# Kernel tuning notes

Hardware: AMD Instinct MI355X
Metric: run time of the kernel (lower is better)

Reference implementation:

```python
import jax, jax.numpy as jnp
import numpy as np

IN_DIM = 6
OUT_DIM = 6
H = 512
OUT_LEN = 256


def _lstm_cell(x, h, c, Wih, Whh, bih, bhh):
    # torch gate order: i, f, g, o
    gates = x @ Wih.T + h @ Whh.T + bih + bhh  # (B, 4H)
    i, f, g, o = jnp.split(gates, 4, axis=-1)
    i = jax.nn.sigmoid(i)
    f = jax.nn.sigmoid(f)
    g = jnp.tanh(g)
    o = jax.nn.sigmoid(o)
    c2 = f * c + i * g
    h2 = o * jnp.tanh(c2)
    return h2, c2


def _lstm_layer(x_seq, Wih, Whh, bih, bhh):
    # x_seq: (T, B, Din) -> (y_seq (T,B,H), h_T (B,H), c_T (B,H))
    B = x_seq.shape[1]
    Hs = Whh.shape[1]
    h0 = jnp.zeros((B, Hs), x_seq.dtype)
    c0 = jnp.zeros((B, Hs), x_seq.dtype)

    def step(carry, x):
        h, c = carry
        h2, c2 = _lstm_cell(x, h, c, Wih, Whh, bih, bhh)
        return (h2, c2), h2

    (hT, cT), ys = jax.lax.scan(step, (h0, c0), x_seq)
    return ys, hT, cT


def setup_inputs() -> dict:
    key = jax.random.key(0)
    ks = jax.random.split(key, 32)
    bound = 1.0 / np.sqrt(H)
    u = lambda k, shape: jax.random.uniform(k, shape, jnp.float32, -bound, bound)
    inp = {"src": jax.random.normal(ks[0], (128, 256, IN_DIM), jnp.float32)}
    # encoder layer 0 / 1
    inp["enc_Wih0"] = u(ks[1], (4 * H, IN_DIM)); inp["enc_Whh0"] = u(ks[2], (4 * H, H))
    inp["enc_bih0"] = u(ks[3], (4 * H,));       inp["enc_bhh0"] = u(ks[4], (4 * H,))
    inp["enc_Wih1"] = u(ks[5], (4 * H, H));     inp["enc_Whh1"] = u(ks[6], (4 * H, H))
    inp["enc_bih1"] = u(ks[7], (4 * H,));       inp["enc_bhh1"] = u(ks[8], (4 * H,))
    # decoder layer 0 / 1
    inp["dec_Wih0"] = u(ks[9], (4 * H, OUT_DIM)); inp["dec_Whh0"] = u(ks[10], (4 * H, H))
    inp["dec_bih0"] = u(ks[11], (4 * H,));        inp["dec_bhh0"] = u(ks[12], (4 * H,))
    inp["dec_Wih1"] = u(ks[13], (4 * H, H));      inp["dec_Whh1"] = u(ks[14], (4 * H, H))
    inp["dec_bih1"] = u(ks[15], (4 * H,));        inp["dec_bhh1"] = u(ks[16], (4 * H,))
    # decoder output head
    inp["fc_W"] = u(ks[17], (OUT_DIM, H))
    inp["fc_b"] = u(ks[18], (OUT_DIM,))
    return inp


def reference(src,
              enc_Wih0, enc_Whh0, enc_bih0, enc_bhh0,
              enc_Wih1, enc_Whh1, enc_bih1, enc_bhh1,
              dec_Wih0, dec_Whh0, dec_bih0, dec_bhh0,
              dec_Wih1, dec_Whh1, dec_bih1, dec_bhh1,
              fc_W, fc_b):
    # ---- encoder: 2-layer unidirectional LSTM over src ----
    x = jnp.transpose(src, (1, 0, 2))  # (Tin, B, 6)
    y0, h0, c0 = _lstm_layer(x, enc_Wih0, enc_Whh0, enc_bih0, enc_bhh0)
    _, h1, c1 = _lstm_layer(y0, enc_Wih1, enc_Whh1, enc_bih1, enc_bhh1)
    # bridge: Henc==Hdec, unidirectional -> identity

    def dec_step(carry, _):
        inp_t, dh0, dc0, dh1, dc1 = carry
        dh0, dc0 = _lstm_cell(inp_t, dh0, dc0, dec_Wih0, dec_Whh0, dec_bih0, dec_bhh0)
        dh1, dc1 = _lstm_cell(dh0, dh1, dc1, dec_Wih1, dec_Whh1, dec_bih1, dec_bhh1)
        out_t = dh1 @ fc_W.T + fc_b  # (B, 6)
        return (out_t, dh0, dc0, dh1, dc1), out_t

    init = (src[:, -1, :], h0, c0, h1, c1)
    _, outs = jax.lax.scan(dec_step, init, None, length=OUT_LEN)
    return jnp.transpose(outs, (1, 0, 2))  # (B, OUT_LEN, 6)
```

## Files before the change

kernel.cpp:

```cpp
#include <hip/hip_runtime.h>
#include <hip/hip_fp16.h>

struct P19 {
  const float *src;
  const float *eWih0, *eWhh0, *ebih0, *ebhh0;
  const float *eWih1, *eWhh1, *ebih1, *ebhh1;
  const float *dWih0, *dWhh0, *dbih0, *dbhh0;
  const float *dWih1, *dWhh1, *dbih1, *dbhh1;
  const float *fcW, *fcb;
  float *out;
  float *ws;
};

typedef _Float16 h2v __attribute__((ext_vector_type(2)));

__device__ __forceinline__ float sigf(float x) { return 1.f / (1.f + __expf(-x)); }

__device__ __forceinline__ unsigned packh(float a, float b2) {
  __half2 h2 = __floats2half2_rn(a, b2);
  return *(const unsigned *)&h2;
}

__device__ __forceinline__ unsigned ldh(const unsigned *p) {
  return __hip_atomic_load((const unsigned *)p, __ATOMIC_RELAXED, __HIP_MEMORY_SCOPE_AGENT);
}
__device__ __forceinline__ void sth(unsigned *p, unsigned v) {
  __hip_atomic_store(p, v, __ATOMIC_RELAXED, __HIP_MEMORY_SCOPE_AGENT);
}
__device__ __forceinline__ void sthf(float *p, float v) {
  __hip_atomic_store(p, v, __ATOMIC_RELAXED, __HIP_MEMORY_SCOPE_AGENT);
}
__device__ __forceinline__ float ldhf(const float *p) {
  return __hip_atomic_load((const float *)p, __ATOMIC_RELAXED, __HIP_MEMORY_SCOPE_AGENT);
}

__device__ __forceinline__ float dot2(unsigned h, unsigned w, float acc) {
#if __has_builtin(__builtin_amdgcn_fdot2)
  return __builtin_amdgcn_fdot2(*(h2v *)&h, *(h2v *)&w, acc, false);
#else
  float2 hf = __half22float2(*(const __half2 *)&h);
  float2 wf = __half22float2(*(const __half2 *)&w);
  return fmaf(hf.x, wf.x, fmaf(hf.y, wf.y, acc));
#endif
}

__device__ __forceinline__ void arrive(unsigned *flags, unsigned gen, int tid, int blk) {
  __syncthreads();
  if (tid == 0) sth(flags + blk * 32, gen);
}
__device__ __forceinline__ void waitbar(unsigned *flags, unsigned gen, int tid) {
  {
    unsigned *f = flags + tid * 32;
    int g = 0;
    while (ldh(f) < gen) {
      __builtin_amdgcn_s_sleep(8);
      if (++g > (1 << 16)) break;
    }
  }
  __syncthreads();
}

__device__ __forceinline__ void dotq1(float *A, const uint4 *__restrict__ wq,
                                      const unsigned *__restrict__ hq) {
  unsigned ca[32], cb[32];
#pragma unroll
  for (int c = 0; c < 32; ++c) ca[c] = ldh(hq + c * 128);
  for (int j = 0; j < 4; j += 2) {
#pragma unroll
    for (int c = 0; c < 32; ++c) cb[c] = ldh(hq + ((j + 1) * 32 + c) * 128);
#pragma unroll
    for (int c = 0; c < 32; ++c) {
      int k2 = j * 32 + c;
      uint4 w0 = wq[k2 * 2], w1 = wq[k2 * 2 + 1];
      unsigned h = ca[c];
      A[0] = dot2(h, w0.x, A[0]); A[1] = dot2(h, w0.y, A[1]);
      A[2] = dot2(h, w0.z, A[2]); A[3] = dot2(h, w0.w, A[3]);
      A[4] = dot2(h, w1.x, A[4]); A[5] = dot2(h, w1.y, A[5]);
      A[6] = dot2(h, w1.z, A[6]); A[7] = dot2(h, w1.w, A[7]);
    }
#pragma unroll
    for (int c = 0; c < 32; ++c) ca[c] = ldh(hq + ((((j + 2) & 3)) * 32 + c) * 128);
#pragma unroll
    for (int c = 0; c < 32; ++c) {
      int k2 = (j + 1) * 32 + c;
      uint4 w0 = wq[k2 * 2], w1 = wq[k2 * 2 + 1];
      unsigned h = cb[c];
      A[0] = dot2(h, w0.x, A[0]); A[1] = dot2(h, w0.y, A[1]);
      A[2] = dot2(h, w0.z, A[2]); A[3] = dot2(h, w0.w, A[3]);
      A[4] = dot2(h, w1.x, A[4]); A[5] = dot2(h, w1.y, A[5]);
      A[6] = dot2(h, w1.z, A[6]); A[7] = dot2(h, w1.w, A[7]);
    }
  }
}
__device__ __forceinline__ void dotq2(float *A, const uint4 *__restrict__ w0q,
                                      const uint4 *__restrict__ w1q,
                                      const unsigned *__restrict__ hq) {
  unsigned ca[32], cb[32];
#pragma unroll
  for (int c = 0; c < 32; ++c) ca[c] = ldh(hq + c * 128);
  for (int j = 0; j < 4; j += 2) {
#pragma unroll
    for (int c = 0; c < 32; ++c) cb[c] = ldh(hq + ((j + 1) * 32 + c) * 128);
#pragma unroll
    for (int c = 0; c < 32; ++c) {
      int k2 = j * 32 + c;
      uint4 a0 = w0q[k2 * 2], a1 = w0q[k2 * 2 + 1];
      uint4 b0 = w1q[k2 * 2], b1 = w1q[k2 * 2 + 1];
      unsigned h = ca[c];
      A[0] = dot2(h, a0.x, A[0]);   A[1] = dot2(h, a0.y, A[1]);
      A[2] = dot2(h, a0.z, A[2]);   A[3] = dot2(h, a0.w, A[3]);
      A[4] = dot2(h, a1.x, A[4]);   A[5] = dot2(h, a1.y, A[5]);
      A[6] = dot2(h, a1.z, A[6]);   A[7] = dot2(h, a1.w, A[7]);
      A[8] = dot2(h, b0.x, A[8]);   A[9] = dot2(h, b0.y, A[9]);
      A[10] = dot2(h, b0.z, A[10]); A[11] = dot2(h, b0.w, A[11]);
      A[12] = dot2(h, b1.x, A[12]); A[13] = dot2(h, b1.y, A[13]);
      A[14] = dot2(h, b1.z, A[14]); A[15] = dot2(h, b1.w, A[15]);
    }
#pragma unroll
    for (int c = 0; c < 32; ++c) ca[c] = ldh(hq + ((((j + 2) & 3)) * 32 + c) * 128);
#pragma unroll
    for (int c = 0; c < 32; ++c) {
      int k2 = (j + 1) * 32 + c;
      uint4 a0 = w0q[k2 * 2], a1 = w0q[k2 * 2 + 1];
      uint4 b0 = w1q[k2 * 2], b1 = w1q[k2 * 2 + 1];
      unsigned h = cb[c];
      A[0] = dot2(h, a0.x, A[0]);   A[1] = dot2(h, a0.y, A[1]);
      A[2] = dot2(h, a0.z, A[2]);   A[3] = dot2(h, a0.w, A[3]);
      A[4] = dot2(h, a1.x, A[4]);   A[5] = dot2(h, a1.y, A[5]);
      A[6] = dot2(h, a1.z, A[6]);   A[7] = dot2(h, a1.w, A[7]);
      A[8] = dot2(h, b0.x, A[8]);   A[9] = dot2(h, b0.y, A[9]);
      A[10] = dot2(h, b0.z, A[10]); A[11] = dot2(h, b0.w, A[11]);
      A[12] = dot2(h, b1.x, A[12]); A[13] = dot2(h, b1.y, A[13]);
      A[14] = dot2(h, b1.z, A[14]); A[15] = dot2(h, b1.w, A[15]);
    }
  }
}

__device__ __forceinline__ void fc_emit(const unsigned *__restrict__ h1buf,
                                        const float *__restrict__ fcW,
                                        const float *__restrict__ fcb,
                                        float *__restrict__ out, int sIdx,
                                        int tid, int blk) {
  int q = tid >> 6, l = tid & 63;
  if (q < 3) {
    int o = blk * 3 + q, j = o >> 7, bb = o & 127;
    const unsigned *hc = h1buf + bb;
    const float2 *fw = (const float2 *)(fcW + j * 512);
    float acc = 0.f;
#pragma unroll
    for (int r = 0; r < 4; ++r) {
      int k2 = l + r * 64;
      unsigned d = ldh(hc + k2 * 128);
      float2 hf = __half22float2(*(const __half2 *)&d);
      float2 wv = fw[k2];
      acc = fmaf(wv.x, hf.x, acc);
      acc = fmaf(wv.y, hf.y, acc);
    }
#pragma unroll
    for (int off = 32; off; off >>= 1) acc += __shfl_down(acc, off, 64);
    if (l == 0) out[((size_t)bb * 256 + sIdx) * 6 + j] = acc + fcb[j];
  }
}

__global__ __launch_bounds__(256, 1) void seq2seq_kernel(P19 p) {
  const int tid = threadIdx.x;
  const int blk = blockIdx.x;
  const int b = tid & 127;
  const int kh = tid >> 7;

  float *ws = p.ws;
  unsigned *flags = (unsigned *)ws;
  unsigned *hpB = (unsigned *)(ws + 8256);
  unsigned *hp0r[2] = {hpB, hpB + 32768};
  unsigned *hp1r[2] = {hpB + 65536, hpB + 98304};
  float *outp = ws + 8256 + 131072;
  float *srcT = outp + 768;

  __shared__ __align__(16) uint4 wl4[3584];
  __shared__ float4 redux[6][128];
  __shared__ float wxe[48], wxd[48], bbuf[40];
  unsigned *wl1 = (unsigned *)wl4;

  {
    const float *mats[6] = {p.eWhh0, p.eWih1, p.eWhh1, p.dWhh0, p.dWih1, p.dWhh1};
    for (int e = tid; e < 12288; e += 256) {
      int k2 = e & 255, r = e >> 8;
      int g = r & 3, uu = (r >> 2) & 1, m = r >> 3;
      const float *row = mats[m] + (size_t)(g * 512 + blk * 2 + uu) * 512;
      wl1[(m * 512 + k2 * 2 + uu) * 4 + g] = packh(row[2 * k2], row[2 * k2 + 1]);
    }
    for (int e = tid; e < 2048; e += 256) {
      int uu = e >> 10, rem = e & 1023, g = rem & 3, k2 = rem >> 2;
      const float *wr = p.dWih0 + (size_t)(g * 512 + blk * 2 + uu) * 6;
      float v0 = 0.f, v1 = 0.f;
#pragma unroll
      for (int i = 0; i < 6; ++i) {
        v0 = fmaf(wr[i], p.fcW[i * 512 + 2 * k2], v0);
        v1 = fmaf(wr[i], p.fcW[i * 512 + 2 * k2 + 1], v1);
      }
      wl1[(6 * 512 + k2 * 2 + uu) * 4 + g] = packh(v0, v1);
    }
    if (tid < 40) {
      int f = tid >> 3, k = tid & 7, uu = k >> 2, g = k & 3;
      int r2 = g * 512 + blk * 2 + uu;
      float v;
      if (f == 0) v = p.ebih0[r2] + p.ebhh0[r2];
      else if (f == 1) v = p.ebih1[r2] + p.ebhh1[r2];
      else if (f == 2) v = p.dbih1[r2] + p.dbhh1[r2];
      else {
        v = p.dbih0[r2] + p.dbhh0[r2];
        if (f == 3)
#pragma unroll
          for (int i = 0; i < 6; ++i) v = fmaf(p.dWih0[(size_t)r2 * 6 + i], p.fcb[i], v);
      }
      bbuf[tid] = v;
    } else if (tid >= 64 && tid < 112) {
      int idx = tid - 64, uu = idx / 24, rem = idx % 24, g = rem / 6, i = rem % 6;
      wxe[idx] = p.eWih0[(size_t)(g * 512 + blk * 2 + uu) * 6 + i];
    } else if (tid >= 128 && tid < 176) {
      int idx = tid - 128, uu = idx / 24, rem = idx % 24, g = rem / 6, i = rem % 6;
      wxd[idx] = p.dWih0[(size_t)(g * 512 + blk * 2 + uu) * 6 + i];
    }
  }
  for (int e = blk * 256 + tid; e < 196608; e += 65536) {
    int bb = e & 127, rest = e >> 7, i = rest % 6, t = rest / 6;
    sthf(&srcT[t * 768 + i * 128 + bb], p.src[((size_t)bb * 256 + t) * 6 + i]);
  }
  {
    int g0 = blk * 256 + tid;
    if (g0 < 768) {
      int bb = g0 & 127, i = g0 >> 7;
      sthf(&outp[i * 128 + bb], p.src[((size_t)bb * 256 + 255) * 6 + i]);
    }
  }
  float c0[2] = {0.f, 0.f}, c1[2] = {0.f, 0.f};
  unsigned gen = 1;
  arrive(flags, gen, tid, blk);
  waitbar(flags, gen, tid);

#define WQ(m) (wl4 + (m) * 512 + kh * 256)
#define HST(buf) ((const unsigned *)(buf) + kh * 16384 + b)
#define RADD(gb, slot) { float4 v = redux[slot][b]; \
    G[(gb)] += v.x; G[(gb) + 1] += v.y; G[(gb) + 2] += v.z; G[(gb) + 3] += v.w; }

  for (int t = 0; t <= 256; ++t) {
    float A16[16], A8[8];
#pragma unroll
    for (int i = 0; i < 16; ++i) A16[i] = 0.f;
#pragma unroll
    for (int i = 0; i < 8; ++i) A8[i] = 0.f;
    dotq2(A16, WQ(0), WQ(1), HST(hp0r[t & 1]));
    dotq1(A8, WQ(2), HST(hp1r[(t + 1) & 1]));
    if (kh) {
      redux[0][b] = make_float4(A16[0], A16[1], A16[2], A16[3]);
      redux[1][b] = make_float4(A16[4], A16[5], A16[6], A16[7]);
      redux[2][b] = make_float4(A16[8], A16[9], A16[10], A16[11]);
      redux[3][b] = make_float4(A16[12], A16[13], A16[14], A16[15]);
      redux[4][b] = make_float4(A8[0], A8[1], A8[2], A8[3]);
      redux[5][b] = make_float4(A8[4], A8[5], A8[6], A8[7]);
    }
    __syncthreads();
    if (kh == 0) {
      float G[24];
#pragma unroll
      for (int i = 0; i < 16; ++i) G[i] = A16[i];
#pragma unroll
      for (int i = 0; i < 8; ++i) G[16 + i] = A8[i];
      { RADD(0, 0) RADD(4, 1) RADD(8, 2) RADD(12, 3) RADD(16, 4) RADD(20, 5) }
      if (t < 256) {
        float xv[6], h0v[2];
#pragma unroll
        for (int i = 0; i < 6; ++i) xv[i] = srcT[t * 768 + i * 128 + b];
#pragma unroll
        for (int uu = 0; uu < 2; ++uu) {
          float g4[4];
#pragma unroll
          for (int g = 0; g < 4; ++g) {
            float v = G[uu * 4 + g] + bbuf[uu * 4 + g];
#pragma unroll
            for (int i = 0; i < 6; ++i) v = fmaf(wxe[uu * 24 + g * 6 + i], xv[i], v);
            g4[g] = v;
          }
          float ig = sigf(g4[0]), fg = sigf(g4[1]), gg = tanhf(g4[2]), og = sigf(g4[3]);
          c0[uu] = fg * c0[uu] + ig * gg;
          h0v[uu] = og * tanhf(c0[uu]);
        }
        sth(&hp0r[(t + 1) & 1][blk * 128 + b], packh(h0v[0], h0v[1]));
      }
      if (t >= 1) {
        float h1v[2];
#pragma unroll
        for (int uu = 0; uu < 2; ++uu) {
          float g4[4];
#pragma unroll
          for (int g = 0; g < 4; ++g)
            g4[g] = G[8 + uu * 4 + g] + G[16 + uu * 4 + g] + bbuf[8 + uu * 4 + g];
          float ig = sigf(g4[0]), fg = sigf(g4[1]), gg = tanhf(g4[2]), og = sigf(g4[3]);
          c1[uu] = fg * c1[uu] + ig * gg;
          h1v[uu] = og * tanhf(c1[uu]);
        }
        sth(&hp1r[t & 1][blk * 128 + b], packh(h1v[0], h1v[1]));
      }
    }
    arrive(flags, ++gen, tid, blk);
    waitbar(flags, gen, tid);
  }

  for (int s = 0; s < 256; ++s) {
    float A3[8];
#pragma unroll
    for (int i = 0; i < 8; ++i) A3[i] = 0.f;
    dotq1(A3, WQ(3), HST(hp0r[s & 1]));
    if (s) waitbar(flags, gen, tid);
    float AA[16];
#pragma unroll
    for (int i = 0; i < 16; ++i) AA[i] = 0.f;
    if (s == 0) {
      dotq1(AA + 8, WQ(5), HST(hp1r[0]));
    } else {
      dotq2(AA, WQ(6), WQ(5), HST(hp1r[s & 1]));
      fc_emit(hp1r[s & 1], p.fcW, p.fcb, p.out, s - 1, tid, blk);
    }
    if (kh) {
      redux[0][b] = make_float4(A3[0], A3[1], A3[2], A3[3]);
      redux[1][b] = make_float4(A3[4], A3[5], A3[6], A3[7]);
      redux[2][b] = make_float4(AA[0], AA[1], AA[2], AA[3]);
      redux[3][b] = make_float4(AA[4], AA[5], AA[6], AA[7]);
    }
    __syncthreads();
    if (kh == 0) {
      float G[8];
#pragma unroll
      for (int i = 0; i < 8; ++i) G[i] = A3[i] + AA[i];
      { RADD(0, 0) RADD(4, 1) RADD(0, 2) RADD(4, 3) }
      float bq[8];
      if (s == 0) {
        float xv[6];
#pragma unroll
        for (int i = 0; i < 6; ++i) xv[i] = ldhf(&outp[i * 128 + b]);
#pragma unroll
        for (int k = 0; k < 8; ++k) {
          int uu = k >> 2, g = k & 3;
          float v = bbuf[32 + k];
#pragma unroll
          for (int i = 0; i < 6; ++i) v = fmaf(wxd[uu * 24 + g * 6 + i], xv[i], v);
          bq[k] = v;
        }
      } else {
#pragma unroll
        for (int k = 0; k < 8; ++k) bq[k] = bbuf[24 + k];
      }
      float h0v[2];
#pragma unroll
      for (int uu = 0; uu < 2; ++uu) {
        float ig = sigf(G[uu * 4 + 0] + bq[uu * 4 + 0]);
        float fg = sigf(G[uu * 4 + 1] + bq[uu * 4 + 1]);
        float gg = tanhf(G[uu * 4 + 2] + bq[uu * 4 + 2]);
        float og = sigf(G[uu * 4 + 3] + bq[uu * 4 + 3]);
        c0[uu] = fg * c0[uu] + ig * gg;
        h0v[uu] = og * tanhf(c0[uu]);
      }
      sth(&hp0r[(s + 1) & 1][blk * 128 + b], packh(h0v[0], h0v[1]));
    }
    arrive(flags, ++gen, tid, blk);
    waitbar(flags, gen, tid);
    float A4[8];
#pragma unroll
    for (int i = 0; i < 8; ++i) A4[i] = AA[8 + i];
    dotq1(A4, WQ(4), HST(hp0r[(s + 1) & 1]));
    if (kh) {
      redux[0][b] = make_float4(A4[0], A4[1], A4[2], A4[3]);
      redux[1][b] = make_float4(A4[4], A4[5], A4[6], A4[7]);
    }
    __syncthreads();
    if (kh == 0) {
      float G[8];
#pragma unroll
      for (int i = 0; i < 8; ++i) G[i] = A4[i];
      { RADD(0, 0) RADD(4, 1) }
      float h1v[2];
#pragma unroll
      for (int uu = 0; uu < 2; ++uu) {
        float ig = sigf(G[uu * 4 + 0] + bbuf[16 + uu * 4 + 0]);
        float fg = sigf(G[uu * 4 + 1] + bbuf[16 + uu * 4 + 1]);
        float gg = tanhf(G[uu * 4 + 2] + bbuf[16 + uu * 4 + 2]);
        float og = sigf(G[uu * 4 + 3] + bbuf[16 + uu * 4 + 3]);
        c1[uu] = fg * c1[uu] + ig * gg;
        h1v[uu] = og * tanhf(c1[uu]);
      }
      sth(&hp1r[(s + 1) & 1][blk * 128 + b], packh(h1v[0], h1v[1]));
    }
    arrive(flags, ++gen, tid, blk);
  }
  waitbar(flags, gen, tid);
  fc_emit(hp1r[0], p.fcW, p.fcb, p.out, 255, tid, blk);
}

extern "C" void kernel_launch(void *const *d_in, const int *in_sizes, int n_in,
                              void *d_out, int out_size, void *d_ws, size_t ws_size,
                              hipStream_t stream) {
  (void)in_sizes; (void)n_in; (void)out_size; (void)ws_size;
  P19 p;
  p.src = (const float *)d_in[0];
  p.eWih0 = (const float *)d_in[1];  p.eWhh0 = (const float *)d_in[2];
  p.ebih0 = (const float *)d_in[3];  p.ebhh0 = (const float *)d_in[4];
  p.eWih1 = (const float *)d_in[5];  p.eWhh1 = (const float *)d_in[6];
  p.ebih1 = (const float *)d_in[7];  p.ebhh1 = (const float *)d_in[8];
  p.dWih0 = (const float *)d_in[9];  p.dWhh0 = (const float *)d_in[10];
  p.dbih0 = (const float *)d_in[11]; p.dbhh0 = (const float *)d_in[12];
  p.dWih1 = (const float *)d_in[13]; p.dWhh1 = (const float *)d_in[14];
  p.dbih1 = (const float *)d_in[15]; p.dbhh1 = (const float *)d_in[16];
  p.fcW = (const float *)d_in[17];   p.fcb = (const float *)d_in[18];
  p.out = (float *)d_out;
  p.ws = (float *)d_ws;

  hipMemsetAsync(d_ws, 0, (size_t)(8256 + 4 * 32768) * sizeof(float), stream);
  seq2seq_kernel<<<dim3(256), dim3(256), 0, stream>>>(p);
}
```

Measured before the change: 12.39 ms.

## Remap threads to two batch elements per lane with four-way K split

Each thread now handles two batch columns using 64-bit hidden-state loads, and the K dimension is split across four wavefronts instead of two. Partial sums are reduced through a new shared buffer, with different wavefronts finishing the layer-0 and layer-1 cells so the two run in parallel. The grid barrier wait now polls with a single wavefront checking four flags per lane. The aim is to reuse each weight load across two batch elements and cut global load and barrier traffic, at the cost of more registers and a three-way shared-memory reduction.

Result: slower. 27.52 ms (+122.0%).

```diff
diff --git a/kernel.cpp b/kernel.cpp
--- a/kernel.cpp
+++ b/kernel.cpp
@@ -22,7 +22,7 @@
 }
 
 __device__ __forceinline__ unsigned ldh(const unsigned *p) {
-  return __hip_atomic_load((const unsigned *)p, __ATOMIC_RELAXED, __HIP_MEMORY_SCOPE_AGENT);
+  return __hip_atomic_load(p, __ATOMIC_RELAXED, __HIP_MEMORY_SCOPE_AGENT);
 }
 __device__ __forceinline__ void sth(unsigned *p, unsigned v) {
   __hip_atomic_store(p, v, __ATOMIC_RELAXED, __HIP_MEMORY_SCOPE_AGENT);
@@ -30,8 +30,20 @@
 __device__ __forceinline__ void sthf(float *p, float v) {
   __hip_atomic_store(p, v, __ATOMIC_RELAXED, __HIP_MEMORY_SCOPE_AGENT);
 }
-__device__ __forceinline__ float ldhf(const float *p) {
-  return __hip_atomic_load((const float *)p, __ATOMIC_RELAXED, __HIP_MEMORY_SCOPE_AGENT);
+__device__ __forceinline__ uint2 ldh2(const unsigned *p) {
+  unsigned long long v = __hip_atomic_load((const unsigned long long *)p,
+                                           __ATOMIC_RELAXED, __HIP_MEMORY_SCOPE_AGENT);
+  uint2 r; r.x = (unsigned)v; r.y = (unsigned)(v >> 32); return r;
+}
+__device__ __forceinline__ void sth2(unsigned *p, unsigned lo, unsigned hi) {
+  unsigned long long v = ((unsigned long long)hi << 32) | (unsigned long long)lo;
+  __hip_atomic_store((unsigned long long *)p, v, __ATOMIC_RELAXED, __HIP_MEMORY_SCOPE_AGENT);
+}
+__device__ __forceinline__ float2 ldhf2(const float *p) {
+  union { unsigned long long u; float2 f; } c;
+  c.u = __hip_atomic_load((const unsigned long long *)p, __ATOMIC_RELAXED,
+                          __HIP_MEMORY_SCOPE_AGENT);
+  return c.f;
 }
 
 __device__ __forceinline__ float dot2(unsigned h, unsigned w, float acc) {
@@ -49,91 +61,119 @@
   if (tid == 0) sth(flags + blk * 32, gen);
 }
 __device__ __forceinline__ void waitbar(unsigned *flags, unsigned gen, int tid) {
-  {
-    unsigned *f = flags + tid * 32;
-    int g = 0;
-    while (ldh(f) < gen) {
-      __builtin_amdgcn_s_sleep(8);
+  if ((tid >> 6) == 3) {
+    int l = tid & 63, g = 0;
+    for (;;) {
+      unsigned a = ldh(flags + (4 * l + 0) * 32);
+      unsigned b = ldh(flags + (4 * l + 1) * 32);
+      unsigned c = ldh(flags + (4 * l + 2) * 32);
+      unsigned d = ldh(flags + (4 * l + 3) * 32);
+      if (min(min(a, b), min(c, d)) >= gen) break;
+      __builtin_amdgcn_s_sleep(4);
       if (++g > (1 << 16)) break;
     }
   }
   __syncthreads();
 }
 
-__device__ __forceinline__ void dotq1(float *A, const uint4 *__restrict__ wq,
+#define DOT8(B, h, w0, w1) {                                          \
+  (B)[0] = dot2(h.x, w0.x, (B)[0]);   (B)[1] = dot2(h.y, w0.x, (B)[1]);   \
+  (B)[2] = dot2(h.x, w0.y, (B)[2]);   (B)[3] = dot2(h.y, w0.y, (B)[3]);   \
+  (B)[4] = dot2(h.x, w0.z, (B)[4]);   (B)[5] = dot2(h.y, w0.z, (B)[5]);   \
+  (B)[6] = dot2(h.x, w0.w, (B)[6]);   (B)[7] = dot2(h.y, w0.w, (B)[7]);   \
+  (B)[8] = dot2(h.x, w1.x, (B)[8]);   (B)[9] = dot2(h.y, w1.x, (B)[9]);   \
+  (B)[10] = dot2(h.x, w1.y, (B)[10]); (B)[11] = dot2(h.y, w1.y, (B)[11]); \
+  (B)[12] = dot2(h.x, w1.z, (B)[12]); (B)[13] = dot2(h.y, w1.z, (B)[13]); \
+  (B)[14] = dot2(h.x, w1.w, (B)[14]); (B)[15] = dot2(h.y, w1.w, (B)[15]); }
+
+__device__ __forceinline__ void dotp1(float *A, const uint4 *__restrict__ wq,
                                       const unsigned *__restrict__ hq) {
-  unsigned ca[32], cb[32];
-#pragma unroll
-  for (int c = 0; c < 32; ++c) ca[c] = ldh(hq + c * 128);
+  uint2 ca[16], cb[16];
+#pragma unroll
+  for (int c = 0; c < 16; ++c) ca[c] = ldh2(hq + c * 128);
   for (int j = 0; j < 4; j += 2) {
 #pragma unroll
-    for (int c = 0; c < 32; ++c) cb[c] = ldh(hq + ((j + 1) * 32 + c) * 128);
-#pragma unroll
-    for (int c = 0; c < 32; ++c) {
-      int k2 = j * 32 + c;
+    for (int c = 0; c < 16; ++c) cb[c] = ldh2(hq + ((j + 1) * 16 + c) * 128);
+#pragma unroll
+    for (int c = 0; c < 16; ++c) {
+      int k2 = j * 16 + c;
       uint4 w0 = wq[k2 * 2], w1 = wq[k2 * 2 + 1];
-      unsigned h = ca[c];
-      A[0] = dot2(h, w0.x, A[0]); A[1] = dot2(h, w0.y, A[1]);
-      A[2] = dot2(h, w0.z, A[2]); A[3] = dot2(h, w0.w, A[3]);
-      A[4] = dot2(h, w1.x, A[4]); A[5] = dot2(h, w1.y, A[5]);
-      A[6] = dot2(h, w1.z, A[6]); A[7] = dot2(h, w1.w, A[7]);
-    }
-#pragma unroll
-    for (int c = 0; c < 32; ++c) ca[c] = ldh(hq + ((((j + 2) & 3)) * 32 + c) * 128);
-#pragma unroll
-    for (int c = 0; c < 32; ++c) {
-      int k2 = (j + 1) * 32 + c;
+      uint2 h = ca[c];
+      DOT8(A, h, w0, w1)
+    }
+#pragma unroll
+    for (int c = 0; c < 16; ++c) ca[c] = ldh2(hq + ((((j + 2) & 3)) * 16 + c) * 128);
+#pragma unroll
+    for (int c = 0; c < 16; ++c) {
+      int k2 = (j + 1) * 16 + c;
       uint4 w0 = wq[k2 * 2], w1 = wq[k2 * 2 + 1];
-      unsigned h = cb[c];
-      A[0] = dot2(h, w0.x, A[0]); A[1] = dot2(h, w0.y, A[1]);
-      A[2] = dot2(h, w0.z, A[2]); A[3] = dot2(h, w0.w, A[3]);
-      A[4] = dot2(h, w1.x, A[4]); A[5] = dot2(h, w1.y, A[5]);
-      A[6] = dot2(h, w1.z, A[6]); A[7] = dot2(h, w1.w, A[7]);
-    }
-  }
-}
-__device__ __forceinline__ void dotq2(float *A, const uint4 *__restrict__ w0q,
-                                      const uint4 *__restrict__ w1q,
+      uint2 h = cb[c];
+      DOT8(A, h, w0, w1)
+    }
+  }
+}
+__device__ __forceinline__ void dotp2(float *A , const uint4 *__restrict__ wa,
+                                      const uint4 *__restrict__ wb,
                                       const unsigned *__restrict__ hq) {
-  unsigned ca[32], cb[32];
-#pragma unroll
-  for (int c = 0; c < 32; ++c) ca[c] = ldh(hq + c * 128);
+  uint2 ca[16], cb[16];
+#pragma unroll
+  for (int c = 0; c < 16; ++c) ca[c] = ldh2(hq + c * 128);
   for (int j = 0; j < 4; j += 2) {
 #pragma unroll
-    for (int c = 0; c < 32; ++c) cb[c] = ldh(hq + ((j + 1) * 32 + c) * 128);
-#pragma unroll
-    for (int c = 0; c < 32; ++c) {
-      int k2 = j * 32 + c;
-      uint4 a0 = w0q[k2 * 2], a1 = w0q[k2 * 2 + 1];
-      uint4 b0 = w1q[k2 * 2], b1 = w1q[k2 * 2 + 1];
-      unsigned h = ca[c];
-      A[0] = dot2(h, a0.x, A[0]);   A[1] = dot2(h, a0.y, A[1]);
-      A[2] = dot2(h, a0.z, A[2]);   A[3] = dot2(h, a0.w, A[3]);
-      A[4] = dot2(h, a1.x, A[4]);   A[5] = dot2(h, a1.y, A[5]);
-      A[6] = dot2(h, a1.z, A[6]);   A[7] = dot2(h, a1.w, A[7]);
-      A[8] = dot2(h, b0.x, A[8]);   A[9] = dot2(h, b0.y, A[9]);
-      A[10] = dot2(h, b0.z, A[10]); A[11] = dot2(h, b0.w, A[11]);
-      A[12] = dot2(h, b1.x, A[12]); A[13] = dot2(h, b1.y, A[13]);
-      A[14] = dot2(h, b1.z, A[14]); A[15] = dot2(h, b1.w, A[15]);
-    }
-#pragma unroll
-    for (int c = 0; c < 32; ++c) ca[c] = ldh(hq + ((((j + 2) & 3)) * 32 + c) * 128);
-#pragma unroll
-    for (int c = 0; c < 32; ++c) {
-      int k2 = (j + 1) * 32 + c;
-      uint4 a0 = w0q[k2 * 2], a1 = w0q[k2 * 2 + 1];
-      uint4 b0 = w1q[k2 * 2], b1 = w1q[k2 * 2 + 1];
-      unsigned h = cb[c];
-      A[0] = dot2(h, a0.x, A[0]);   A[1] = dot2(h, a0.y, A[1]);
-      A[2] = dot2(h, a0.z, A[2]);   A[3] = dot2(h, a0.w, A[3]);
-      A[4] = dot2(h, a1.x, A[4]);   A[5] = dot2(h, a1.y, A[5]);
-      A[6] = dot2(h, a1.z, A[6]);   A[7] = dot2(h, a1.w, A[7]);
-      A[8] = dot2(h, b0.x, A[8]);   A[9] = dot2(h, b0.y, A[9]);
-      A[10] = dot2(h, b0.z, A[10]); A[11] = dot2(h, b0.w, A[11]);
-      A[12] = dot2(h, b1.x, A[12]); A[13] = dot2(h, b1.y, A[13]);
-      A[14] = dot2(h, b1.z, A[14]); A[15] = dot2(h, b1.w, A[15]);
-    }
-  }
+    for (int c = 0; c < 16; ++c) cb[c] = ldh2(hq + ((j + 1) * 16 + c) * 128);
+#pragma unroll
+    for (int c = 0; c < 16; ++c) {
+      int k2 = j * 16 + c;
+      uint2 h = ca[c];
+      uint4 w0 = wa[k2 * 2], w1 = wa[k2 * 2 + 1];
+      DOT8(A, h, w0, w1)
+      uint4 v0 = wb[k2 * 2], v1 = wb[k2 * 2 + 1];
+      DOT8(A + 16, h, v0, v1)
+    }
+#pragma unroll
+    for (int c = 0; c < 16; ++c) ca[c] = ldh2(hq + ((((j + 2) & 3)) * 16 + c) * 128);
+#pragma unroll
+    for (int c = 0; c < 16; ++c) {
+      int k2 = (j + 1) * 16 + c;
+      uint2 h = cb[c];
+      uint4 w0 = wa[k2 * 2], w1 = wa[k2 * 2 + 1];
+      DOT8(A, h, w0, w1)
+      uint4 v0 = wb[k2 * 2], v1 = wb[k2 * 2 + 1];
+      DOT8(A + 16, h, v0, v1)
+    }
+  }
+}
+
+__device__ __forceinline__ void rwrite(float *dst, const float *A) {
+#pragma unroll
+  for (int q = 0; q < 4; ++q)
+    *(float4 *)&dst[q * 4] = make_float4(A[q * 4], A[q * 4 + 1], A[q * 4 + 2], A[q * 4 + 3]);
+}
+__device__ __forceinline__ void rread3(float (*B)[64][20], int l, float *G) {
+#pragma unroll
+  for (int wi = 0; wi < 3; ++wi)
+#pragma unroll
+    for (int q = 0; q < 4; ++q) {
+      float4 v = *(const float4 *)&B[wi][l][q * 4];
+      G[q * 4] += v.x; G[q * 4 + 1] += v.y; G[q * 4 + 2] += v.z; G[q * 4 + 3] += v.w;
+    }
+}
+
+__device__ __forceinline__ void cell2(const float *G, float c[2][2], unsigned hv[2]) {
+  float h[2][2];
+#pragma unroll
+  for (int u = 0; u < 2; ++u)
+#pragma unroll
+    for (int p = 0; p < 2; ++p) {
+      float ig = sigf(G[u * 8 + 0 + p]);
+      float fg = sigf(G[u * 8 + 2 + p]);
+      float gg = tanhf(G[u * 8 + 4 + p]);
+      float og = sigf(G[u * 8 + 6 + p]);
+      c[u][p] = fg * c[u][p] + ig * gg;
+      h[u][p] = og * tanhf(c[u][p]);
+    }
+  hv[0] = packh(h[0][0], h[1][0]);
+  hv[1] = packh(h[0][1], h[1][1]);
 }
 
 __device__ __forceinline__ void fc_emit(const unsigned *__restrict__ h1buf,
@@ -165,8 +205,8 @@
 __global__ __launch_bounds__(256, 1) void seq2seq_kernel(P19 p) {
   const int tid = threadIdx.x;
   const int blk = blockIdx.x;
-  const int b = tid & 127;
-  const int kh = tid >> 7;
+  const int w = tid >> 6;
+  const int l = tid & 63;
 
   float *ws = p.ws;
   unsigned *flags = (unsigned *)ws;
@@ -177,7 +217,7 @@
   float *srcT = outp + 768;
 
   __shared__ __align__(16) uint4 wl4[3584];
-  __shared__ float4 redux[6][128];
+  __shared__ __align__(16) float rb[3][3][64][20];
   __shared__ float wxe[48], wxd[48], bbuf[40];
   unsigned *wl1 = (unsigned *)wl4;
 
@@ -233,162 +273,164 @@
       sthf(&outp[i * 128 + bb], p.src[((size_t)bb * 256 + 255) * 6 + i]);
     }
   }
-  float c0[2] = {0.f, 0.f}, c1[2] = {0.f, 0.f};
+  float c0[2][2] = {{0.f, 0.f}, {0.f, 0.f}};
+  float c1[2][2] = {{0.f, 0.f}, {0.f, 0.f}};
   unsigned gen = 1;
   arrive(flags, gen, tid, blk);
   waitbar(flags, gen, tid);
 
-#define WQ(m) (wl4 + (m) * 512 + kh * 256)
-#define HST(buf) ((const unsigned *)(buf) + kh * 16384 + b)
-#define RADD(gb, slot) { float4 v = redux[slot][b]; \
-    G[(gb)] += v.x; G[(gb) + 1] += v.y; G[(gb) + 2] += v.z; G[(gb) + 3] += v.w; }
+#define WQn(m) (wl4 + (m) * 512 + w * 128)
+#define HSTn(buf) ((const unsigned *)(buf) + w * 8192 + 2 * l)
 
   for (int t = 0; t <= 256; ++t) {
-    float A16[16], A8[8];
-#pragma unroll
-    for (int i = 0; i < 16; ++i) A16[i] = 0.f;
-#pragma unroll
-    for (int i = 0; i < 8; ++i) A8[i] = 0.f;
-    dotq2(A16, WQ(0), WQ(1), HST(hp0r[t & 1]));
-    dotq1(A8, WQ(2), HST(hp1r[(t + 1) & 1]));
-    if (kh) {
-      redux[0][b] = make_float4(A16[0], A16[1], A16[2], A16[3]);
-      redux[1][b] = make_float4(A16[4], A16[5], A16[6], A16[7]);
-      redux[2][b] = make_float4(A16[8], A16[9], A16[10], A16[11]);
-      redux[3][b] = make_float4(A16[12], A16[13], A16[14], A16[15]);
-      redux[4][b] = make_float4(A8[0], A8[1], A8[2], A8[3]);
-      redux[5][b] = make_float4(A8[4], A8[5], A8[6], A8[7]);
+    float A2[32], A1[16];
+#pragma unroll
+    for (int i = 0; i < 32; ++i) A2[i] = 0.f;
+#pragma unroll
+    for (int i = 0; i < 16; ++i) A1[i] = 0.f;
+    dotp2(A2, WQn(0), WQn(1), HSTn(hp0r[t & 1]));
+    dotp1(A1, WQn(2), HSTn(hp1r[(t + 1) & 1]));
+    if (w != 0) rwrite(&rb[0][w - 1][l][0], A2);
+    if (w != 2) {
+      int wi = w > 2 ? w - 1 : w;
+      rwrite(&rb[1][wi][l][0], A2 + 16);
+      rwrite(&rb[2][wi][l][0], A1);
     }
     __syncthreads();
-    if (kh == 0) {
-      float G[24];
-#pragma unroll
-      for (int i = 0; i < 16; ++i) G[i] = A16[i];
-#pragma unroll
-      for (int i = 0; i < 8; ++i) G[16 + i] = A8[i];
-      { RADD(0, 0) RADD(4, 1) RADD(8, 2) RADD(12, 3) RADD(16, 4) RADD(20, 5) }
-      if (t < 256) {
-        float xv[6], h0v[2];
-#pragma unroll
-        for (int i = 0; i < 6; ++i) xv[i] = srcT[t * 768 + i * 128 + b];
-#pragma unroll
-        for (int uu = 0; uu < 2; ++uu) {
-          float g4[4];
-#pragma unroll
-          for (int g = 0; g < 4; ++g) {
-            float v = G[uu * 4 + g] + bbuf[uu * 4 + g];
-#pragma unroll
-            for (int i = 0; i < 6; ++i) v = fmaf(wxe[uu * 24 + g * 6 + i], xv[i], v);
-            g4[g] = v;
+    if (w == 0 && t < 256) {
+      float G[16];
+#pragma unroll
+      for (int i = 0; i < 16; ++i) G[i] = A2[i];
+      rread3(rb[0], l, G);
+      float2 xv[6];
+#pragma unroll
+      for (int i = 0; i < 6; ++i)
+        xv[i] = *(const float2 *)&srcT[t * 768 + i * 128 + 2 * l];
+#pragma unroll
+      for (int u = 0; u < 2; ++u)
+#pragma unroll
+        for (int g = 0; g < 4; ++g) {
+          float a0 = bbuf[u * 4 + g], a1 = a0;
+#pragma unroll
+          for (int i = 0; i < 6; ++i) {
+            float wv = wxe[u * 24 + g * 6 + i];
+            a0 = fmaf(wv, xv[i].x, a0);
+            a1 = fmaf(wv, xv[i].y, a1);
           }
-          float ig = sigf(g4[0]), fg = sigf(g4[1]), gg = tanhf(g4[2]), og = sigf(g4[3]);
-          c0[uu] = fg * c0[uu] + ig * gg;
-          h0v[uu] = og * tanhf(c0[uu]);
+          G[u * 8 + g * 2 + 0] += a0;
+          G[u * 8 + g * 2 + 1] += a1;
         }
-        sth(&hp0r[(t + 1) & 1][blk * 128 + b], packh(h0v[0], h0v[1]));
-      }
-      if (t >= 1) {
-        float h1v[2];
-#pragma unroll
-        for (int uu = 0; uu < 2; ++uu) {
-          float g4[4];
-#pragma unroll
-          for (int g = 0; g < 4; ++g)
-            g4[g] = G[8 + uu * 4 + g] + G[16 + uu * 4 + g] + bbuf[8 + uu * 4 + g];
-          float ig = sigf(g4[0]), fg = sigf(g4[1]), gg = tanhf(g4[2]), og = sigf(g4[3]);
-          c1[uu] = fg * c1[uu] + ig * gg;
-          h1v[uu] = og * tanhf(c1[uu]);
+      unsigned hv[2];
+      cell2(G, c0, hv);
+      sth2(&hp0r[(t + 1) & 1][blk * 128 + 2 * l], hv[0], hv[1]);
+    }
+    if (w == 2 && t >= 1) {
+      float G[16];
+#pragma unroll
+      for (int i = 0; i < 16; ++i) G[i] = A2[16 + i] + A1[i];
+      rread3(rb[1], l, G);
+      rread3(rb[2], l, G);
+#pragma unroll
+      for (int u = 0; u < 2; ++u)
+#pragma unroll
+        for (int g = 0; g < 4; ++g) {
+          float bs = bbuf[8 + u * 4 + g];
+          G[u * 8 + g * 2 + 0] += bs;
+          G[u * 8 + g * 2 + 1] += bs;
         }
-        sth(&hp1r[t & 1][blk * 128 + b], packh(h1v[0], h1v[1]));
-      }
+      unsigned hv[2];
+      cell2(G, c1, hv);
+      sth2(&hp1r[t & 1][blk * 128 + 2 * l], hv[0], hv[1]);
     }
     arrive(flags, ++gen, tid, blk);
     waitbar(flags, gen, tid);
   }
 
   for (int s = 0; s < 256; ++s) {
-    float A3[8];
-#pragma unroll
-    for (int i = 0; i < 8; ++i) A3[i] = 0.f;
-    dotq1(A3, WQ(3), HST(hp0r[s & 1]));
+    float A0[16];
+#pragma unroll
+    for (int i = 0; i < 16; ++i) A0[i] = 0.f;
+    dotp1(A0, WQn(3), HSTn(hp0r[s & 1]));
     if (s) waitbar(flags, gen, tid);
-    float AA[16];
-#pragma unroll
-    for (int i = 0; i < 16; ++i) AA[i] = 0.f;
+    float A12[32];
+#pragma unroll
+    for (int i = 0; i < 32; ++i) A12[i] = 0.f;
     if (s == 0) {
-      dotq1(AA + 8, WQ(5), HST(hp1r[0]));
+      dotp1(A12 + 16, WQn(5), HSTn(hp1r[0]));
     } else {
-      dotq2(AA, WQ(6), WQ(5), HST(hp1r[s & 1]));
+      dotp2(A12, WQn(6), WQn(5), HSTn(hp1r[s & 1]));
       fc_emit(hp1r[s & 1], p.fcW, p.fcb, p.out, s - 1, tid, blk);
     }
-    if (kh) {
-      redux[0][b] = make_float4(A3[0], A3[1], A3[2], A3[3]);
-      redux[1][b] = make_float4(A3[4], A3[5], A3[6], A3[7]);
-      redux[2][b] = make_float4(AA[0], AA[1], AA[2], AA[3]);
-      redux[3][b] = make_float4(AA[4], AA[5], AA[6], AA[7]);
+    if (w != 0) {
+      rwrite(&rb[0][w - 1][l][0], A0);
+      rwrite(&rb[1][w - 1][l][0], A12);
     }
     __syncthreads();
-    if (kh == 0) {
-      float G[8];
-#pragma unroll
-      for (int i = 0; i < 8; ++i) G[i] = A3[i] + AA[i];
-      { RADD(0, 0) RADD(4, 1) RADD(0, 2) RADD(4, 3) }
-      float bq[8];
+    if (w == 0) {
+      float G[16];
+#pragma unroll
+      for (int i = 0; i < 16; ++i) G[i] = A0[i] + A12[i];
+      rread3(rb[0], l, G);
+      rread3(rb[1], l, G);
       if (s == 0) {
-        float xv[6];
-#pragma unroll
-        for (int i = 0; i < 6; ++i) xv[i] = ldhf(&outp[i * 128 + b]);
-#pragma unroll
-        for (int k = 0; k < 8; ++k) {
-          int uu = k >> 2, g = k & 3;
-          float v = bbuf[32 + k];
-#pragma unroll
-          for (int i = 0; i < 6; ++i) v = fmaf(wxd[uu * 24 + g * 6 + i], xv[i], v);
-          bq[k] = v;
-        }
+        float2 xv[6];
+#pragma unroll
+        for (int i = 0; i < 6; ++i) xv[i] = ldhf2(&outp[i * 128 + 2 * l]);
+#pragma unroll
+        for (int u = 0; u < 2; ++u)
+#pragma unroll
+          for (int g = 0; g < 4; ++g) {
+            float a0 = bbuf[32 + u * 4 + g], a1 = a0;
+#pragma unroll
+            for (int i = 0; i < 6; ++i) {
+              float wv = wxd[u * 24 + g * 6 + i];
+              a0 = fmaf(wv, xv[i].x, a0);
+              a1 = fmaf(wv, xv[i].y, a1);
+            }
+            G[u * 8 + g * 2 + 0] += a0;
+            G[u * 8 + g * 2 + 1] += a1;
+          }
       } else {
 #pragma unroll
-        for (int k = 0; k < 8; ++k) bq[k] = bbuf[24 + k];
+        for (int u = 0; u < 2; ++u)
+#pragma unroll
+          for (int g = 0; g < 4; ++g) {
+            float bs = bbuf[24 + u * 4 + g];
+            G[u * 8 + g * 2 + 0] += bs;
+            G[u * 8 + g * 2 + 1] += bs;
+          }
       }
-      float h0v[2];
-#pragma unroll
-      for (int uu = 0; uu < 2; ++uu) {
-        float ig = sigf(G[uu * 4 + 0] + bq[uu * 4 + 0]);
-        float fg = sigf(G[uu * 4 + 1] + bq[uu * 4 + 1]);
-        float gg = tanhf(G[uu * 4 + 2] + bq[uu * 4 + 2]);
-        float og = sigf(G[uu * 4 + 3] + bq[uu * 4 + 3]);
-        c0[uu] = fg * c0[uu] + ig * gg;
-        h0v[uu] = og * tanhf(c0[uu]);
-      }
-      sth(&hp0r[(s + 1) & 1][blk * 128 + b], packh(h0v[0], h0v[1]));
+      unsigned hv[2];
+      cell2(G, c0, hv);
+      sth2(&hp0r[(s + 1) & 1][blk * 128 + 2 * l], hv[0], hv[1]);
     }
     arrive(flags, ++gen, tid, blk);
     waitbar(flags, gen, tid);
-    float A4[8];
-#pragma unroll
-    for (int i = 0; i < 8; ++i) A4[i] = AA[8 + i];
-    dotq1(A4, WQ(4), HST(hp0r[(s + 1) & 1]));
-    if (kh) {
-      redux[0][b] = make_float4(A4[0], A4[1], A4[2], A4[3]);
-      redux[1][b] = make_float4(A4[4], A4[5], A4[6], A4[7]);
+    float A4[16];
+#pragma unroll
+    for (int i = 0; i < 16; ++i) A4[i] = A12[16 + i];
+    dotp1(A4, WQn(4), HSTn(hp0r[(s + 1) & 1]));
+    if (w != 2) {
+      int wi = w > 2 ? w - 1 : w;
+      rwrite(&rb[2][wi][l][0], A4);
     }
     __syncthreads();
-    if (kh == 0) {
-      float G[8];
-#pragma unroll
-      for (int i = 0; i < 8; ++i) G[i] = A4[i];
-      { RADD(0, 0) RADD(4, 1) }
-      float h1v[2];
-#pragma unroll
-      for (int uu = 0; uu < 2; ++uu) {
-        float ig = sigf(G[uu * 4 + 0] + bbuf[16 + uu * 4 + 0]);
-        float fg = sigf(G[uu * 4 + 1] + bbuf[16 + uu * 4 + 1]);
-        float gg = tanhf(G[uu * 4 + 2] + bbuf[16 + uu * 4 + 2]);
-        float og = sigf(G[uu * 4 + 3] + bbuf[16 + uu * 4 + 3]);
-        c1[uu] = fg * c1[uu] + ig * gg;
-        h1v[uu] = og * tanhf(c1[uu]);
-      }
-      sth(&hp1r[(s + 1) & 1][blk * 128 + b], packh(h1v[0], h1v[1]));
+    if (w == 2) {
+      float G[16];
+#pragma unroll
+      for (int i = 0; i < 16; ++i) G[i] = A4[i];
+      rread3(rb[2], l, G);
+#pragma unroll
+      for (int u = 0; u < 2; ++u)
+#pragma unroll
+        for (int g = 0; g < 4; ++g) {
+          float bs = bbuf[16 + u * 4 + g];
+          G[u * 8 + g * 2 + 0] += bs;
+          G[u * 8 + g * 2 + 1] += bs;
+        }
+      unsigned hv[2];
+      cell2(G, c1, hv);
+      sth2(&hp1r[(s + 1) & 1][blk * 128 + 2 * l], hv[0], hv[1]);
     }
     arrive(flags, ++gen, tid, blk);
   }
```
